# Kernel tuning notes

Hardware: AMD Instinct MI355X
Metric: run time of the kernel (lower is better)

## Reference

```python
import jax, jax.numpy as jnp
import numpy as np

N = 50000      # nodes
E = 1600000    # edges
IN = 128       # in_feats
H = 4          # heads
F = 32         # per-head feats (h_feats = out_feats = 32)
NEG_SLOPE = 0.2


def setup_inputs() -> dict:
    key = jax.random.key(0)
    ks = jax.random.split(key, 12)
    glorot = lambda k, shape: jax.random.normal(k, shape, jnp.float32) * np.sqrt(2.0 / (shape[0] + shape[-1])).astype(np.float32)
    x = jax.random.normal(ks[0], (N, IN), jnp.float32)
    edge_index = jax.random.randint(ks[1], (2, E), 0, N, dtype=jnp.int32)
    W1 = glorot(ks[2], (IN, H * F))
    att_src1 = glorot(ks[3], (H, F))
    att_dst1 = glorot(ks[4], (H, F))
    b1 = jnp.zeros((F,), jnp.float32)
    W2 = glorot(ks[5], (F, H * F))
    att_src2 = glorot(ks[6], (H, F))
    att_dst2 = glorot(ks[7], (H, F))
    b2 = jnp.zeros((F,), jnp.float32)
    return {"x": x, "edge_index": edge_index,
            "W1": W1, "att_src1": att_src1, "att_dst1": att_dst1, "b1": b1,
            "W2": W2, "att_src2": att_src2, "att_dst2": att_dst2, "b2": b2}


def gat_conv(x, edge_index, W, a_src, a_dst, bias):
    """PyG GATConv with concat=False (head-average), add_self_loops=True."""
    n = x.shape[0]
    h = (x @ W).reshape(n, H, F)                      # [N,H,F]
    loops = jnp.arange(n, dtype=edge_index.dtype)
    src = jnp.concatenate([edge_index[0], loops])     # [E+N]
    dst = jnp.concatenate([edge_index[1], loops])
    alpha_src = jnp.einsum('nhf,hf->nh', h, a_src)    # [N,H]
    alpha_dst = jnp.einsum('nhf,hf->nh', h, a_dst)
    e = jax.nn.leaky_relu(alpha_src[src] + alpha_dst[dst], NEG_SLOPE)  # [E+N,H]
    # scatter-softmax over incoming edges per destination node
    m = jax.ops.segment_max(e, dst, num_segments=n)
    e = jnp.exp(e - m[dst])
    s = jax.ops.segment_sum(e, dst, num_segments=n)
    alpha = e / (s[dst] + 1e-16)                      # [E+N,H]
    out = jax.ops.segment_sum(alpha[:, :, None] * h[src], dst, num_segments=n)  # [N,H,F]
    return out.mean(axis=1) + bias                    # concat=False: average heads


def reference(x, edge_index, W1, att_src1, att_dst1, b1, W2, att_src2, att_dst2, b2):
    h = gat_conv(x, edge_index, W1, att_src1, att_dst1, b1)
    h = jax.nn.elu(h)
    return gat_conv(h, edge_index, W2, att_src2, att_dst2, b2)
```

## Files before the change

### kernel.cpp

```cpp
#include <hip/hip_runtime.h>
#include <hip/hip_bf16.h>
#include <hip/hip_fp16.h>
#include <math.h>


#define NS 32
#define NB 8
#define MAXNPB 8192

__device__ __forceinline__ float lrelu(float x) { return x > 0.f ? x : 0.2f * x; }

__device__ __forceinline__ unsigned int fenc(float f) {
    unsigned int u = __float_as_uint(f);
    return (u & 0x80000000u) ? ~u : (u | 0x80000000u);
}
__device__ __forceinline__ float fdec(unsigned int e) {
    unsigned int u = (e & 0x80000000u) ? (e & 0x7FFFFFFFu) : ~e;
    return __uint_as_float(u);
}

__device__ __forceinline__ unsigned short f2bf(float x) {
    unsigned u = __float_as_uint(x);
    return (unsigned short)((u + 0x7FFFu + ((u >> 16) & 1u)) >> 16);
}
__device__ __forceinline__ float bflo(unsigned w) { return __uint_as_float(w << 16); }
__device__ __forceinline__ float bfhi(unsigned w) { return __uint_as_float(w & 0xFFFF0000u); }

__device__ __forceinline__ unsigned pack_h2(float a, float b) {
    const __half2 h = __float22half2_rn(make_float2(a, b));
    return *(const unsigned*)&h;
}
__device__ __forceinline__ float2 unpack_h2(unsigned w) {
    __half2 h = *(const __half2*)&w;
    return __half22float2(h);
}

__global__ __launch_bounds__(256) void hist_kernel(
    const int* __restrict__ dst, int* __restrict__ cnt_priv,
    int E, int n, int npb) {
    __shared__ int h[MAXNPB];
    const int b = blockIdx.x & (NB - 1);
    const int s = blockIdx.x / NB;
    const int lo = b * npb;
    const int hi = min(lo + npb, n);
    const int span = hi - lo;
    if (span <= 0) return;
    for (int j = threadIdx.x; j < span; j += 256) h[j] = 0;
    __syncthreads();
    const int E4 = E >> 2;
    const int len4 = (E4 + NS - 1) / NS;
    const int beg4 = s * len4;
    const int end4 = min(beg4 + len4, E4);
    const int4* dst4 = (const int4*)dst;
    for (int i = beg4 + threadIdx.x; i < end4; i += 256) {
        const int4 d = dst4[i];
        if (d.x >= lo && d.x < hi) atomicAdd(&h[d.x - lo], 1);
        if (d.y >= lo && d.y < hi) atomicAdd(&h[d.y - lo], 1);
        if (d.z >= lo && d.z < hi) atomicAdd(&h[d.z - lo], 1);
        if (d.w >= lo && d.w < hi) atomicAdd(&h[d.w - lo], 1);
    }
    if (s == NS - 1) {
        for (int i = (E4 << 2) + threadIdx.x; i < E; i += 256) {
            const int d = dst[i];
            if (d >= lo && d < hi) atomicAdd(&h[d - lo], 1);
        }
    }
    __syncthreads();
    int* outp = cnt_priv + (size_t)s * n + lo;
    for (int j = threadIdx.x; j < span; j += 256) outp[j] = h[j];
}

__global__ __launch_bounds__(256) void scan_part(int* __restrict__ cnt_priv,
                                                 int* __restrict__ deg,
                                                 int* __restrict__ bsum, int n) {
    __shared__ int red[256];
    const int t = threadIdx.x;
    const int node = blockIdx.x * 256 + t;
    int run = 0;
    if (node < n) {
#pragma unroll 4
        for (int s = 0; s < NS; ++s) {
            int* p = &cnt_priv[(size_t)s * n + node];
            const int c = *p;
            *p = run;
            run += c;
        }
        deg[node] = run;
    }
    red[t] = (node < n) ? run : 0;
    __syncthreads();
    for (int o = 128; o > 0; o >>= 1) {
        if (t < o) red[t] += red[t + o];
        __syncthreads();
    }
    if (t == 0) bsum[blockIdx.x] = red[0];
}

__global__ __launch_bounds__(256) void scan_mid(const int* __restrict__ bsum,
                                                int* __restrict__ boff, int nb,
                                                int* __restrict__ rowptr, int n) {
    __shared__ int s[256];
    const int t = threadIdx.x;
    const int v = (t < nb) ? bsum[t] : 0;
    s[t] = v;
    __syncthreads();
    for (int o = 1; o < 256; o <<= 1) {
        const int u = (t >= o) ? s[t - o] : 0;
        __syncthreads();
        s[t] += u;
        __syncthreads();
    }
    if (t < nb) boff[t] = s[t] - v;
    if (t == 255) rowptr[n] = s[255];
}

__global__ __launch_bounds__(256) void scan_final(const int* __restrict__ deg,
                                                  const int* __restrict__ boff,
                                                  int* __restrict__ rowptr, int n) {
    __shared__ int s[256];
    const int t = threadIdx.x;
    const int i = blockIdx.x * 256 + t;
    const int v = (i < n) ? deg[i] : 0;
    s[t] = v;
    __syncthreads();
    for (int o = 1; o < 256; o <<= 1) {
        const int u = (t >= o) ? s[t - o] : 0;
        __syncthreads();
        s[t] += u;
        __syncthreads();
    }
    if (i < n) rowptr[i] = boff[blockIdx.x] + s[t] - v;
}

__global__ __launch_bounds__(256) void scatter_kernel(
    const int* __restrict__ src, const int* __restrict__ dst,
    const int* __restrict__ rowptr, const int* __restrict__ cnt_priv,
    unsigned long long* __restrict__ sd, int E, int n, int npb) {
    __shared__ int cur[MAXNPB];
    const int b = blockIdx.x & (NB - 1);
    const int s = blockIdx.x / NB;
    const int lo = b * npb;
    const int hi = min(lo + npb, n);
    const int span = hi - lo;
    if (span <= 0) return;
    {
        const int* cp = cnt_priv + (size_t)s * n + lo;
        const int* rp = rowptr + lo;
        for (int j = threadIdx.x; j < span; j += 256) cur[j] = rp[j] + cp[j];
    }
    __syncthreads();
    const int E4 = E >> 2;
    const int len4 = (E4 + NS - 1) / NS;
    const int beg4 = s * len4;
    const int end4 = min(beg4 + len4, E4);
    const int4* dst4 = (const int4*)dst;
    const int4* src4 = (const int4*)src;
    for (int i = beg4 + threadIdx.x; i < end4; i += 256) {
        const int4 d = dst4[i];
        const int4 sv = src4[i];
        if (d.x >= lo && d.x < hi) {
            const int p = atomicAdd(&cur[d.x - lo], 1);
            sd[p] = ((unsigned long long)(unsigned)(d.x << 4) << 32) | (unsigned)(sv.x << 4);
        }
        if (d.y >= lo && d.y < hi) {
            const int p = atomicAdd(&cur[d.y - lo], 1);
            sd[p] = ((unsigned long long)(unsigned)(d.y << 4) << 32) | (unsigned)(sv.y << 4);
        }
        if (d.z >= lo && d.z < hi) {
            const int p = atomicAdd(&cur[d.z - lo], 1);
            sd[p] = ((unsigned long long)(unsigned)(d.z << 4) << 32) | (unsigned)(sv.z << 4);
        }
        if (d.w >= lo && d.w < hi) {
            const int p = atomicAdd(&cur[d.w - lo], 1);
            sd[p] = ((unsigned long long)(unsigned)(d.w << 4) << 32) | (unsigned)(sv.w << 4);
        }
    }
    if (s == NS - 1) {
        for (int i = (E4 << 2) + threadIdx.x; i < E; i += 256) {
            const int d = dst[i];
            if (d >= lo && d < hi) {
                const int p = atomicAdd(&cur[d - lo], 1);
                sd[p] = ((unsigned long long)(unsigned)(d << 4) << 32) | (unsigned)(src[i] << 4);
            }
        }
    }
}

__global__ __launch_bounds__(256) void edge_w_kernel(
    const unsigned long long* __restrict__ sd,
    const float* __restrict__ asrc, const float* __restrict__ adst,
    const unsigned int* __restrict__ gmax, unsigned long long* __restrict__ wq,
    int Etot) {
    const char* aB = (const char*)asrc;
    const char* dB = (const char*)adst;
    const float g0 = fdec(gmax[0]), g1 = fdec(gmax[1]);
    const float g2 = fdec(gmax[2]), g3 = fdec(gmax[3]);
    for (int i = blockIdx.x * blockDim.x + threadIdx.x; i < Etot;
         i += gridDim.x * blockDim.x) {
        const unsigned long long rec = __builtin_nontemporal_load(&sd[i]);
        const unsigned s16 = (unsigned)rec;
        const unsigned d16 = (unsigned)(rec >> 32);
        const float4 as = *(const float4*)(aB + s16);
        const float4 ad = *(const float4*)(dB + d16);
        const float q0 = __expf(lrelu(as.x + ad.x) - lrelu(g0 + ad.x));
        const float q1 = __expf(lrelu(as.y + ad.y) - lrelu(g1 + ad.y));
        const float q2 = __expf(lrelu(as.z + ad.z) - lrelu(g2 + ad.z));
        const float q3 = __expf(lrelu(as.w + ad.w) - lrelu(g3 + ad.w));
        const unsigned lo = pack_h2(q0, q1);
        const unsigned hi = pack_h2(q2, q3);
        const unsigned long long out = ((unsigned long long)hi << 32) | lo;
        __builtin_nontemporal_store(out, &wq[i]);
    }
}

template <int K>
__global__ __launch_bounds__(256) void gemm_kernel(
    const float* __restrict__ X, const float* __restrict__ W,
    const float* __restrict__ AttS, const float* __restrict__ AttD,
    unsigned short* __restrict__ Hb, float* __restrict__ asrc, float* __restrict__ adst,
    unsigned int* __restrict__ gmax, int n) {
    constexpr int KC = 32;
    __shared__ __align__(16) float Ws[KC * 128];
    __shared__ __align__(16) float Xs[64 * K];
    __shared__ unsigned int smax[4];
    const int tid = threadIdx.x;

    const int r = tid >> 5;
    const int sub = tid & 31;
    const int head = sub >> 3;
    const int pos = ((head & 1) << 1) | (head >> 1);
    const int fc = (sub & 7) * 4;
    const int rowBase = blockIdx.x * 64;

    if (tid < 4) smax[tid] = 0u;
    {
        const float4* X4 = (const float4*)X;
        float4* Xs4 = (float4*)Xs;
        const int K4 = K / 4;
        for (int i = tid; i < 64 * K4; i += 256) {
            int rr = rowBase + i / K4;
            Xs4[i] = (rr < n) ? X4[(size_t)rr * K4 + (i % K4)] : make_float4(0.f, 0.f, 0.f, 0.f);
        }
    }

    float acc[8][4] = {};
    const float4* Ws4 = (const float4*)Ws;
    for (int kt = 0; kt < K; kt += KC) {
        __syncthreads();
        {
            const float4* W4 = (const float4*)(W + kt * 128);
            float4* WsS = (float4*)Ws;
#pragma unroll
            for (int i = 0; i < 4; ++i) WsS[tid + i * 256] = W4[tid + i * 256];
        }
        __syncthreads();
#pragma unroll
        for (int k = 0; k < KC; k += 4) {
            float4 wv[4];
#pragma unroll
            for (int j = 0; j < 4; ++j) wv[j] = Ws4[(k + j) * 32 + sub];
            float4 xv[8];
#pragma unroll
            for (int b = 0; b < 8; ++b)
                xv[b] = *(const float4*)&Xs[(b * 8 + r) * K + kt + k];
#pragma unroll
            for (int b = 0; b < 8; ++b) {
                acc[b][0] = fmaf(xv[b].x, wv[0].x, acc[b][0]);
                acc[b][1] = fmaf(xv[b].x, wv[0].y, acc[b][1]);
                acc[b][2] = fmaf(xv[b].x, wv[0].z, acc[b][2]);
                acc[b][3] = fmaf(xv[b].x, wv[0].w, acc[b][3]);
                acc[b][0] = fmaf(xv[b].y, wv[1].x, acc[b][0]);
                acc[b][1] = fmaf(xv[b].y, wv[1].y, acc[b][1]);
                acc[b][2] = fmaf(xv[b].y, wv[1].z, acc[b][2]);
                acc[b][3] = fmaf(xv[b].y, wv[1].w, acc[b][3]);
                acc[b][0] = fmaf(xv[b].z, wv[2].x, acc[b][0]);
                acc[b][1] = fmaf(xv[b].z, wv[2].y, acc[b][1]);
                acc[b][2] = fmaf(xv[b].z, wv[2].z, acc[b][2]);
                acc[b][3] = fmaf(xv[b].z, wv[2].w, acc[b][3]);
                acc[b][0] = fmaf(xv[b].w, wv[3].x, acc[b][0]);
                acc[b][1] = fmaf(xv[b].w, wv[3].y, acc[b][1]);
                acc[b][2] = fmaf(xv[b].w, wv[3].z, acc[b][2]);
                acc[b][3] = fmaf(xv[b].w, wv[3].w, acc[b][3]);
            }
        }
    }

    float a_s[4], a_d[4];
#pragma unroll
    for (int j = 0; j < 4; ++j) {
        a_s[j] = AttS[head * 32 + fc + j];
        a_d[j] = AttD[head * 32 + fc + j];
    }
#pragma unroll
    for (int b = 0; b < 8; ++b) {
        const int row = rowBase + b * 8 + r;
        const float p0 = __shfl_xor(acc[b][0], 16);
        const float p1 = __shfl_xor(acc[b][1], 16);
        const float p2 = __shfl_xor(acc[b][2], 16);
        const float p3 = __shfl_xor(acc[b][3], 16);
        if (row < n) {
            if (head < 2) {
                uint4 o;
                o.x = (unsigned)f2bf(acc[b][0]) | ((unsigned)f2bf(p0) << 16);
                o.y = (unsigned)f2bf(acc[b][1]) | ((unsigned)f2bf(p1) << 16);
                o.z = (unsigned)f2bf(acc[b][2]) | ((unsigned)f2bf(p2) << 16);
                o.w = (unsigned)f2bf(acc[b][3]) | ((unsigned)f2bf(p3) << 16);
                *(uint4*)((char*)Hb + (size_t)row * 256 + head * 128 + fc * 4) = o;
            }
            float ps = acc[b][0] * a_s[0] + acc[b][1] * a_s[1] +
                       acc[b][2] * a_s[2] + acc[b][3] * a_s[3];
            float pd = acc[b][0] * a_d[0] + acc[b][1] * a_d[1] +
                       acc[b][2] * a_d[2] + acc[b][3] * a_d[3];
#pragma unroll
            for (int msk = 1; msk < 8; msk <<= 1) {
                ps += __shfl_xor(ps, msk);
                pd += __shfl_xor(pd, msk);
            }
            if ((sub & 7) == 0) {
                asrc[row * 4 + pos] = ps;
                adst[row * 4 + pos] = pd;
                atomicMax(&smax[pos], fenc(ps));
            }
        }
    }
    __syncthreads();
    if (tid < 4) atomicMax(&gmax[tid], smax[tid]);
}

__global__ __launch_bounds__(256) void node_kernel(
    const int* __restrict__ rowptr, const unsigned long long* __restrict__ sd,
    const unsigned short* __restrict__ Hb, const float* __restrict__ asrc,
    const float* __restrict__ adst, const unsigned int* __restrict__ gmax,
    const unsigned long long* __restrict__ wq, const float* __restrict__ bias,
    float* __restrict__ outp, int n, int apply_elu) {
    const int node = blockIdx.x * 4 + (threadIdx.x >> 6);
    if (node >= n) return;
    const int lane = threadIdx.x & 63;
    const unsigned f = lane & 31;
    const unsigned hp = lane >> 5;
    const unsigned hp8 = hp * 8;
    const unsigned hp4 = hp * 4;
    const unsigned hpf = hp * 128 + f * 4;
    const unsigned node16 = (unsigned)node * 16;
    const char* aB = (const char*)asrc;
    const char* dB = (const char*)adst;
    const char* hB = (const char*)Hb;
    const char* wB = (const char*)wq;

    const int beg = rowptr[node], end = rowptr[node + 1];
    const float2 ad01 = *(const float2*)(dB + node16 + hp8);
    const float2 M01 = make_float2(lrelu(fdec(gmax[hp * 2]) + ad01.x),
                                   lrelu(fdec(gmax[hp * 2 + 1]) + ad01.y));

    const float2 aself = *(const float2*)(aB + node16 + hp8);
    float2 q = make_float2(__expf(lrelu(aself.x + ad01.x) - M01.x),
                           __expf(lrelu(aself.y + ad01.y) - M01.y));
    float2 s01 = q;
    const unsigned wSelf = *(const unsigned*)(hB + (node16 << 4) + hpf);
    float2 acc01 = make_float2(q.x * bflo(wSelf), q.y * bfhi(wSelf));

    int i = beg;
    for (; i + 16 <= end; i += 16) {
        unsigned sx[16];
#pragma unroll
        for (int u = 0; u < 16; ++u)
            sx[u] = (unsigned)__builtin_nontemporal_load(&sd[i + u]);
        unsigned wv[16];
#pragma unroll
        for (int u = 0; u < 16; ++u)
            wv[u] = *(const unsigned*)(wB + (((unsigned)(i + u)) << 3) + hp4);
        unsigned w[16];
#pragma unroll
        for (int u = 0; u < 16; ++u) w[u] = *(const unsigned*)(hB + (sx[u] << 4) + hpf);
#pragma unroll
        for (int u = 0; u < 16; ++u) {
            const float2 qf = unpack_h2(wv[u]);
            s01.x += qf.x; s01.y += qf.y;
            acc01.x = fmaf(qf.x, bflo(w[u]), acc01.x);
            acc01.y = fmaf(qf.y, bfhi(w[u]), acc01.y);
        }
    }
    for (; i + 4 <= end; i += 4) {
        unsigned sx[4];
#pragma unroll
        for (int u = 0; u < 4; ++u)
            sx[u] = (unsigned)__builtin_nontemporal_load(&sd[i + u]);
        unsigned wv[4];
#pragma unroll
        for (int u = 0; u < 4; ++u)
            wv[u] = *(const unsigned*)(wB + (((unsigned)(i + u)) << 3) + hp4);
        unsigned w[4];
#pragma unroll
        for (int u = 0; u < 4; ++u) w[u] = *(const unsigned*)(hB + (sx[u] << 4) + hpf);
#pragma unroll
        for (int u = 0; u < 4; ++u) {
            const float2 qf = unpack_h2(wv[u]);
            s01.x += qf.x; s01.y += qf.y;
            acc01.x = fmaf(qf.x, bflo(w[u]), acc01.x);
            acc01.y = fmaf(qf.y, bfhi(w[u]), acc01.y);
        }
    }
    for (; i < end; ++i) {
        const unsigned sx = (unsigned)__builtin_nontemporal_load(&sd[i]);
        const unsigned wh = *(const unsigned*)(wB + (((unsigned)i) << 3) + hp4);
        const unsigned wv = *(const unsigned*)(hB + (sx << 4) + hpf);
        const float2 qf = unpack_h2(wh);
        s01.x += qf.x; s01.y += qf.y;
        acc01.x = fmaf(qf.x, bflo(wv), acc01.x);
        acc01.y = fmaf(qf.y, bfhi(wv), acc01.y);
    }

    float v = acc01.x / s01.x + acc01.y / s01.y;
    v += __shfl_xor(v, 32);
    v = v * 0.25f + bias[f];
    if (apply_elu) v = (v > 0.f) ? v : (__expf(v) - 1.f);
    if (lane < 32) outp[(size_t)node * 32 + f] = v;
}


extern "C" void kernel_launch(void* const* d_in, const int* in_sizes, int n_in,
                              void* d_out, int out_size, void* d_ws, size_t ws_size,
                              hipStream_t stream) {
    const int N = in_sizes[0] / 128;
    const int E = in_sizes[1] / 2;
    const float* x = (const float*)d_in[0];
    const int* ei = (const int*)d_in[1];
    const float* W1 = (const float*)d_in[2];
    const float* atS1 = (const float*)d_in[3];
    const float* atD1 = (const float*)d_in[4];
    const float* b1 = (const float*)d_in[5];
    const float* W2 = (const float*)d_in[6];
    const float* atS2 = (const float*)d_in[7];
    const float* atD2 = (const float*)d_in[8];
    const float* b2 = (const float*)d_in[9];
    float* out = (float*)d_out;

    char* ws = (char*)d_ws;
    size_t off = 0;
    auto alloc = [&](size_t bytes) {
        void* p = ws + off;
        off = (off + bytes + 255) & ~(size_t)255;
        return p;
    };
    unsigned int* gmax = (unsigned int*)alloc(8 * sizeof(unsigned int));
    int* cnt_priv = (int*)alloc((size_t)NS * N * 4);
    int* deg = (int*)alloc((size_t)N * 4);
    int* rowptr = (int*)alloc((size_t)(N + 1) * 4);
    int* bsum = (int*)alloc(256 * 4);
    int* boff = (int*)alloc(256 * 4);
    unsigned long long* sd = (unsigned long long*)alloc((size_t)E * 8);
    unsigned long long* wq = (unsigned long long*)alloc((size_t)E * 8);
    unsigned short* hb = (unsigned short*)alloc((size_t)N * 128 * 2);
    float* av_s = (float*)alloc((size_t)N * 4 * 4);
    float* av_d = (float*)alloc((size_t)N * 4 * 4);
    float* x2 = (float*)alloc((size_t)N * 32 * 4);

    const int* e_src = ei;
    const int* e_dst = ei + E;

    const int gemmGrid = (N + 63) / 64;
    const int nodeGrid = (N + 3) / 4;
    const int npb = (N + NB - 1) / NB;
    const int scanGrid = (N + 255) / 256;
    const int bsGrid = NB * NS;

    (void)hipMemsetAsync(gmax, 0, 8 * sizeof(unsigned int), stream);

    hist_kernel<<<bsGrid, 256, 0, stream>>>(e_dst, cnt_priv, E, N, npb);
    scan_part<<<scanGrid, 256, 0, stream>>>(cnt_priv, deg, bsum, N);
    scan_mid<<<1, 256, 0, stream>>>(bsum, boff, scanGrid, rowptr, N);
    scan_final<<<scanGrid, 256, 0, stream>>>(deg, boff, rowptr, N);
    scatter_kernel<<<bsGrid, 256, 0, stream>>>(e_src, e_dst, rowptr, cnt_priv, sd, E, N, npb);

    gemm_kernel<128><<<gemmGrid, 256, 0, stream>>>(
        x, W1, atS1, atD1, hb, av_s, av_d, gmax, N);
    edge_w_kernel<<<2048, 256, 0, stream>>>(sd, av_s, av_d, gmax, wq, E);
    node_kernel<<<nodeGrid, 256, 0, stream>>>(rowptr, sd, hb, av_s, av_d, gmax,
                                              wq, b1, x2, N, 1);
    gemm_kernel<32><<<gemmGrid, 256, 0, stream>>>(
        x2, W2, atS2, atD2, hb, av_s, av_d, gmax + 4, N);
    edge_w_kernel<<<2048, 256, 0, stream>>>(sd, av_s, av_d, gmax + 4, wq, E);
    node_kernel<<<nodeGrid, 256, 0, stream>>>(rowptr, sd, hb, av_s, av_d, gmax + 4,
                                              wq, b2, out, N, 0);
}
```

Baseline: 373.2 us.

## Fuse layer-1 edge weights into scatter and interleave edge records with weights

Moves the scatter kernel after the first GEMM so it can compute the layer-1 attention weights while placing each edge. This removes one edge_w pass and one re-read of the sorted edge list. Source index, destination and fp16 weights now sit in one 16-byte record per edge, and the second-layer edge_w kernel writes its weights into that record in place. The bf16 feature layout becomes head-interleaved, so the node kernel can use 32 lanes per node, each covering all four heads with one 8-byte gather, and the head-pair shuffle goes away. It also doubles NS, which enlarges the private histogram and the scatter grid, and the scatter kernel now does extra gathers and exp work.

```diff
diff --git a/kernel.cpp b/kernel.cpp
--- a/kernel.cpp
+++ b/kernel.cpp
@@ -4,7 +4,7 @@
 #include <math.h>
 
 
-#define NS 32
+#define NS 64
 #define NB 8
 #define MAXNPB 8192
 
@@ -135,7 +135,9 @@
 __global__ __launch_bounds__(256) void scatter_kernel(
     const int* __restrict__ src, const int* __restrict__ dst,
     const int* __restrict__ rowptr, const int* __restrict__ cnt_priv,
-    unsigned long long* __restrict__ sd, int E, int n, int npb) {
+    const float* __restrict__ asrc, const float* __restrict__ adst,
+    const unsigned int* __restrict__ gmax,
+    uint4* __restrict__ esd, int E, int n, int npb) {
     __shared__ int cur[MAXNPB];
     const int b = blockIdx.x & (NB - 1);
     const int s = blockIdx.x / NB;
@@ -149,6 +151,24 @@
         for (int j = threadIdx.x; j < span; j += 256) cur[j] = rp[j] + cp[j];
     }
     __syncthreads();
+    const char* aB = (const char*)asrc;
+    const char* dB = (const char*)adst;
+    const float g0 = fdec(gmax[0]), g1 = fdec(gmax[1]);
+    const float g2 = fdec(gmax[2]), g3 = fdec(gmax[3]);
+
+    auto place = [&](int sv, int dv) {
+        const int p = atomicAdd(&cur[dv - lo], 1);
+        const unsigned s16 = (unsigned)(sv << 4);
+        const unsigned d16 = (unsigned)(dv << 4);
+        const float4 as = *(const float4*)(aB + s16);
+        const float4 ad = *(const float4*)(dB + d16);
+        const float q0 = __expf(lrelu(as.x + ad.x) - lrelu(g0 + ad.x));
+        const float q1 = __expf(lrelu(as.y + ad.y) - lrelu(g1 + ad.y));
+        const float q2 = __expf(lrelu(as.z + ad.z) - lrelu(g2 + ad.z));
+        const float q3 = __expf(lrelu(as.w + ad.w) - lrelu(g3 + ad.w));
+        esd[p] = make_uint4(s16, d16, pack_h2(q0, q1), pack_h2(q2, q3));
+    };
+
     const int E4 = E >> 2;
     const int len4 = (E4 + NS - 1) / NS;
     const int beg4 = s * len4;
@@ -158,58 +178,43 @@
     for (int i = beg4 + threadIdx.x; i < end4; i += 256) {
         const int4 d = dst4[i];
         const int4 sv = src4[i];
-        if (d.x >= lo && d.x < hi) {
-            const int p = atomicAdd(&cur[d.x - lo], 1);
-            sd[p] = ((unsigned long long)(unsigned)(d.x << 4) << 32) | (unsigned)(sv.x << 4);
-        }
-        if (d.y >= lo && d.y < hi) {
-            const int p = atomicAdd(&cur[d.y - lo], 1);
-            sd[p] = ((unsigned long long)(unsigned)(d.y << 4) << 32) | (unsigned)(sv.y << 4);
-        }
-        if (d.z >= lo && d.z < hi) {
-            const int p = atomicAdd(&cur[d.z - lo], 1);
-            sd[p] = ((unsigned long long)(unsigned)(d.z << 4) << 32) | (unsigned)(sv.z << 4);
-        }
-        if (d.w >= lo && d.w < hi) {
-            const int p = atomicAdd(&cur[d.w - lo], 1);
-            sd[p] = ((unsigned long long)(unsigned)(d.w << 4) << 32) | (unsigned)(sv.w << 4);
-        }
+        if (d.x >= lo && d.x < hi) place(sv.x, d.x);
+        if (d.y >= lo && d.y < hi) place(sv.y, d.y);
+        if (d.z >= lo && d.z < hi) place(sv.z, d.z);
+        if (d.w >= lo && d.w < hi) place(sv.w, d.w);
     }
     if (s == NS - 1) {
         for (int i = (E4 << 2) + threadIdx.x; i < E; i += 256) {
             const int d = dst[i];
-            if (d >= lo && d < hi) {
-                const int p = atomicAdd(&cur[d - lo], 1);
-                sd[p] = ((unsigned long long)(unsigned)(d << 4) << 32) | (unsigned)(src[i] << 4);
-            }
+            if (d >= lo && d < hi) place(src[i], d);
         }
     }
 }
 
 __global__ __launch_bounds__(256) void edge_w_kernel(
-    const unsigned long long* __restrict__ sd,
+    uint4* __restrict__ esd,
     const float* __restrict__ asrc, const float* __restrict__ adst,
-    const unsigned int* __restrict__ gmax, unsigned long long* __restrict__ wq,
-    int Etot) {
+    const unsigned int* __restrict__ gmax, int Etot) {
     const char* aB = (const char*)asrc;
     const char* dB = (const char*)adst;
     const float g0 = fdec(gmax[0]), g1 = fdec(gmax[1]);
     const float g2 = fdec(gmax[2]), g3 = fdec(gmax[3]);
     for (int i = blockIdx.x * blockDim.x + threadIdx.x; i < Etot;
          i += gridDim.x * blockDim.x) {
-        const unsigned long long rec = __builtin_nontemporal_load(&sd[i]);
-        const unsigned s16 = (unsigned)rec;
-        const unsigned d16 = (unsigned)(rec >> 32);
+        const unsigned long long sd =
+            __builtin_nontemporal_load((const unsigned long long*)&esd[i]);
+        const unsigned s16 = (unsigned)sd;
+        const unsigned d16 = (unsigned)(sd >> 32);
         const float4 as = *(const float4*)(aB + s16);
         const float4 ad = *(const float4*)(dB + d16);
         const float q0 = __expf(lrelu(as.x + ad.x) - lrelu(g0 + ad.x));
         const float q1 = __expf(lrelu(as.y + ad.y) - lrelu(g1 + ad.y));
         const float q2 = __expf(lrelu(as.z + ad.z) - lrelu(g2 + ad.z));
         const float q3 = __expf(lrelu(as.w + ad.w) - lrelu(g3 + ad.w));
-        const unsigned lo = pack_h2(q0, q1);
-        const unsigned hi = pack_h2(q2, q3);
-        const unsigned long long out = ((unsigned long long)hi << 32) | lo;
-        __builtin_nontemporal_store(out, &wq[i]);
+        const unsigned long long rec =
+            ((unsigned long long)pack_h2(q2, q3) << 32) | pack_h2(q0, q1);
+        __builtin_nontemporal_store(
+            rec, (unsigned long long*)((char*)&esd[i] + 8));
     }
 }
 
@@ -300,12 +305,11 @@
         const float p3 = __shfl_xor(acc[b][3], 16);
         if (row < n) {
             if (head < 2) {
-                uint4 o;
-                o.x = (unsigned)f2bf(acc[b][0]) | ((unsigned)f2bf(p0) << 16);
-                o.y = (unsigned)f2bf(acc[b][1]) | ((unsigned)f2bf(p1) << 16);
-                o.z = (unsigned)f2bf(acc[b][2]) | ((unsigned)f2bf(p2) << 16);
-                o.w = (unsigned)f2bf(acc[b][3]) | ((unsigned)f2bf(p3) << 16);
-                *(uint4*)((char*)Hb + (size_t)row * 256 + head * 128 + fc * 4) = o;
+                char* base = (char*)Hb + (size_t)row * 256 + (unsigned)fc * 8 + head * 4;
+                *(unsigned*)(base + 0)  = (unsigned)f2bf(acc[b][0]) | ((unsigned)f2bf(p0) << 16);
+                *(unsigned*)(base + 8)  = (unsigned)f2bf(acc[b][1]) | ((unsigned)f2bf(p1) << 16);
+                *(unsigned*)(base + 16) = (unsigned)f2bf(acc[b][2]) | ((unsigned)f2bf(p2) << 16);
+                *(unsigned*)(base + 24) = (unsigned)f2bf(acc[b][3]) | ((unsigned)f2bf(p3) << 16);
             }
             float ps = acc[b][0] * a_s[0] + acc[b][1] * a_s[1] +
                        acc[b][2] * a_s[2] + acc[b][3] * a_s[3];
@@ -328,93 +332,77 @@
 }
 
 __global__ __launch_bounds__(256) void node_kernel(
-    const int* __restrict__ rowptr, const unsigned long long* __restrict__ sd,
+    const int* __restrict__ rowptr, const uint4* __restrict__ esd,
     const unsigned short* __restrict__ Hb, const float* __restrict__ asrc,
     const float* __restrict__ adst, const unsigned int* __restrict__ gmax,
-    const unsigned long long* __restrict__ wq, const float* __restrict__ bias,
+    const float* __restrict__ bias,
     float* __restrict__ outp, int n, int apply_elu) {
-    const int node = blockIdx.x * 4 + (threadIdx.x >> 6);
+    const int node = blockIdx.x * 8 + (threadIdx.x >> 5);
     if (node >= n) return;
-    const int lane = threadIdx.x & 63;
-    const unsigned f = lane & 31;
-    const unsigned hp = lane >> 5;
-    const unsigned hp8 = hp * 8;
-    const unsigned hp4 = hp * 4;
-    const unsigned hpf = hp * 128 + f * 4;
-    const unsigned node16 = (unsigned)node * 16;
-    const char* aB = (const char*)asrc;
-    const char* dB = (const char*)adst;
+    const unsigned f = threadIdx.x & 31;
+    const unsigned f8 = f * 8;
     const char* hB = (const char*)Hb;
-    const char* wB = (const char*)wq;
+    const unsigned long long* eB = (const unsigned long long*)esd;
 
     const int beg = rowptr[node], end = rowptr[node + 1];
-    const float2 ad01 = *(const float2*)(dB + node16 + hp8);
-    const float2 M01 = make_float2(lrelu(fdec(gmax[hp * 2]) + ad01.x),
-                                   lrelu(fdec(gmax[hp * 2 + 1]) + ad01.y));
-
-    const float2 aself = *(const float2*)(aB + node16 + hp8);
-    float2 q = make_float2(__expf(lrelu(aself.x + ad01.x) - M01.x),
-                           __expf(lrelu(aself.y + ad01.y) - M01.y));
-    float2 s01 = q;
-    const unsigned wSelf = *(const unsigned*)(hB + (node16 << 4) + hpf);
-    float2 acc01 = make_float2(q.x * bflo(wSelf), q.y * bfhi(wSelf));
+    const float4 ad4 = *(const float4*)(adst + (size_t)node * 4);
+    const float4 as4 = *(const float4*)(asrc + (size_t)node * 4);
+    const float M0 = lrelu(fdec(gmax[0]) + ad4.x);
+    const float M1 = lrelu(fdec(gmax[1]) + ad4.y);
+    const float M2 = lrelu(fdec(gmax[2]) + ad4.z);
+    const float M3 = lrelu(fdec(gmax[3]) + ad4.w);
+
+    const float q0 = __expf(lrelu(as4.x + ad4.x) - M0);
+    const float q1 = __expf(lrelu(as4.y + ad4.y) - M1);
+    const float q2 = __expf(lrelu(as4.z + ad4.z) - M2);
+    const float q3 = __expf(lrelu(as4.w + ad4.w) - M3);
+    float s0 = q0, s1 = q1, s2 = q2, s3 = q3;
+    const uint2 hs = *(const uint2*)(hB + ((size_t)node << 8) + f8);
+    float a0 = q0 * bflo(hs.x);
+    float a1 = q1 * bfhi(hs.x);
+    float a2 = q2 * bflo(hs.y);
+    float a3 = q3 * bfhi(hs.y);
 
     int i = beg;
-    for (; i + 16 <= end; i += 16) {
-        unsigned sx[16];
-#pragma unroll
-        for (int u = 0; u < 16; ++u)
-            sx[u] = (unsigned)__builtin_nontemporal_load(&sd[i + u]);
-        unsigned wv[16];
-#pragma unroll
-        for (int u = 0; u < 16; ++u)
-            wv[u] = *(const unsigned*)(wB + (((unsigned)(i + u)) << 3) + hp4);
-        unsigned w[16];
-#pragma unroll
-        for (int u = 0; u < 16; ++u) w[u] = *(const unsigned*)(hB + (sx[u] << 4) + hpf);
-#pragma unroll
-        for (int u = 0; u < 16; ++u) {
-            const float2 qf = unpack_h2(wv[u]);
-            s01.x += qf.x; s01.y += qf.y;
-            acc01.x = fmaf(qf.x, bflo(w[u]), acc01.x);
-            acc01.y = fmaf(qf.y, bfhi(w[u]), acc01.y);
-        }
-    }
-    for (; i + 4 <= end; i += 4) {
-        unsigned sx[4];
-#pragma unroll
-        for (int u = 0; u < 4; ++u)
-            sx[u] = (unsigned)__builtin_nontemporal_load(&sd[i + u]);
-        unsigned wv[4];
-#pragma unroll
-        for (int u = 0; u < 4; ++u)
-            wv[u] = *(const unsigned*)(wB + (((unsigned)(i + u)) << 3) + hp4);
-        unsigned w[4];
-#pragma unroll
-        for (int u = 0; u < 4; ++u) w[u] = *(const unsigned*)(hB + (sx[u] << 4) + hpf);
-#pragma unroll
-        for (int u = 0; u < 4; ++u) {
-            const float2 qf = unpack_h2(wv[u]);
-            s01.x += qf.x; s01.y += qf.y;
-            acc01.x = fmaf(qf.x, bflo(w[u]), acc01.x);
-            acc01.y = fmaf(qf.y, bfhi(w[u]), acc01.y);
+    for (; i + 8 <= end; i += 8) {
+        unsigned long long e0[8], e1[8];
+#pragma unroll
+        for (int u = 0; u < 8; ++u) {
+            e0[u] = __builtin_nontemporal_load(&eB[(size_t)(i + u) * 2]);
+            e1[u] = __builtin_nontemporal_load(&eB[(size_t)(i + u) * 2 + 1]);
+        }
+        uint2 h[8];
+#pragma unroll
+        for (int u = 0; u < 8; ++u)
+            h[u] = *(const uint2*)(hB + (((unsigned)e0[u]) << 4) + f8);
+#pragma unroll
+        for (int u = 0; u < 8; ++u) {
+            const float2 qa = unpack_h2((unsigned)e1[u]);
+            const float2 qb = unpack_h2((unsigned)(e1[u] >> 32));
+            s0 += qa.x; s1 += qa.y; s2 += qb.x; s3 += qb.y;
+            a0 = fmaf(qa.x, bflo(h[u].x), a0);
+            a1 = fmaf(qa.y, bfhi(h[u].x), a1);
+            a2 = fmaf(qb.x, bflo(h[u].y), a2);
+            a3 = fmaf(qb.y, bfhi(h[u].y), a3);
         }
     }
     for (; i < end; ++i) {
-        const unsigned sx = (unsigned)__builtin_nontemporal_load(&sd[i]);
-        const unsigned wh = *(const unsigned*)(wB + (((unsigned)i) << 3) + hp4);
-        const unsigned wv = *(const unsigned*)(hB + (sx << 4) + hpf);
-        const float2 qf = unpack_h2(wh);
-        s01.x += qf.x; s01.y += qf.y;
-        acc01.x = fmaf(qf.x, bflo(wv), acc01.x);
-        acc01.y = fmaf(qf.y, bfhi(wv), acc01.y);
-    }
-
-    float v = acc01.x / s01.x + acc01.y / s01.y;
-    v += __shfl_xor(v, 32);
+        const unsigned long long e0 = __builtin_nontemporal_load(&eB[(size_t)i * 2]);
+        const unsigned long long e1 = __builtin_nontemporal_load(&eB[(size_t)i * 2 + 1]);
+        const uint2 h = *(const uint2*)(hB + (((unsigned)e0) << 4) + f8);
+        const float2 qa = unpack_h2((unsigned)e1);
+        const float2 qb = unpack_h2((unsigned)(e1 >> 32));
+        s0 += qa.x; s1 += qa.y; s2 += qb.x; s3 += qb.y;
+        a0 = fmaf(qa.x, bflo(h.x), a0);
+        a1 = fmaf(qa.y, bfhi(h.x), a1);
+        a2 = fmaf(qb.x, bflo(h.y), a2);
+        a3 = fmaf(qb.y, bfhi(h.y), a3);
+    }
+
+    float v = a0 / s0 + a1 / s1 + a2 / s2 + a3 / s3;
     v = v * 0.25f + bias[f];
     if (apply_elu) v = (v > 0.f) ? v : (__expf(v) - 1.f);
-    if (lane < 32) outp[(size_t)node * 32 + f] = v;
+    outp[(size_t)node * 32 + f] = v;
 }
 
 
@@ -448,8 +436,7 @@
     int* rowptr = (int*)alloc((size_t)(N + 1) * 4);
     int* bsum = (int*)alloc(256 * 4);
     int* boff = (int*)alloc(256 * 4);
-    unsigned long long* sd = (unsigned long long*)alloc((size_t)E * 8);
-    unsigned long long* wq = (unsigned long long*)alloc((size_t)E * 8);
+    uint4* esd = (uint4*)alloc((size_t)E * 16);
     unsigned short* hb = (unsigned short*)alloc((size_t)N * 128 * 2);
     float* av_s = (float*)alloc((size_t)N * 4 * 4);
     float* av_d = (float*)alloc((size_t)N * 4 * 4);
@@ -459,7 +446,7 @@
     const int* e_dst = ei + E;
 
     const int gemmGrid = (N + 63) / 64;
-    const int nodeGrid = (N + 3) / 4;
+    const int nodeGrid = (N + 7) / 8;
     const int npb = (N + NB - 1) / NB;
     const int scanGrid = (N + 255) / 256;
     const int bsGrid = NB * NS;
@@ -470,16 +457,16 @@
     scan_part<<<scanGrid, 256, 0, stream>>>(cnt_priv, deg, bsum, N);
     scan_mid<<<1, 256, 0, stream>>>(bsum, boff, scanGrid, rowptr, N);
     scan_final<<<scanGrid, 256, 0, stream>>>(deg, boff, rowptr, N);
-    scatter_kernel<<<bsGrid, 256, 0, stream>>>(e_src, e_dst, rowptr, cnt_priv, sd, E, N, npb);
 
     gemm_kernel<128><<<gemmGrid, 256, 0, stream>>>(
         x, W1, atS1, atD1, hb, av_s, av_d, gmax, N);
-    edge_w_kernel<<<2048, 256, 0, stream>>>(sd, av_s, av_d, gmax, wq, E);
-    node_kernel<<<nodeGrid, 256, 0, stream>>>(rowptr, sd, hb, av_s, av_d, gmax,
-                                              wq, b1, x2, N, 1);
+    scatter_kernel<<<bsGrid, 256, 0, stream>>>(
+        e_src, e_dst, rowptr, cnt_priv, av_s, av_d, gmax, esd, E, N, npb);
+    node_kernel<<<nodeGrid, 256, 0, stream>>>(rowptr, esd, hb, av_s, av_d, gmax,
+                                              b1, x2, N, 1);
     gemm_kernel<32><<<gemmGrid, 256, 0, stream>>>(
         x2, W2, atS2, atD2, hb, av_s, av_d, gmax + 4, N);
-    edge_w_kernel<<<2048, 256, 0, stream>>>(sd, av_s, av_d, gmax + 4, wq, E);
-    node_kernel<<<nodeGrid, 256, 0, stream>>>(rowptr, sd, hb, av_s, av_d, gmax + 4,
-                                              wq, b2, out, N, 0);
-}
+    edge_w_kernel<<<2048, 256, 0, stream>>>(esd, av_s, av_d, gmax + 4, E);
+    node_kernel<<<nodeGrid, 256, 0, stream>>>(rowptr, esd, hb, av_s, av_d, gmax + 4,
+                                              b2, out, N, 0);
+}
```

Measured after the change: 365.4 us. 1.02x faster.
